# Optimization experiments

Measured on AMD Instinct MI355X. Metric: run time of the kernel, lower is better.

The kernel has to match this reference:

```python
import jax, jax.numpy as jnp
import numpy as np

BN_EPS = 1e-5

def _conv(x, w, b, pad):
    # x: [B,C,H,W], w: [O,I,kh,kw] -> [B,O,H,W]
    y = jax.lax.conv_general_dilated(x, w, window_strides=(1, 1),
                                     padding=[(pad, pad), (pad, pad)],
                                     dimension_numbers=("NCHW", "OIHW", "NCHW"))
    return y + b[None, :, None, None]

def setup_inputs() -> dict:
    key = jax.random.key(0)
    ks = jax.random.split(key, 5)
    B, Cin, H, W = 2, 256, 80, 80
    Ck, Cv, Cout = 128, 256, 256
    std = 0.02  # matches torch normal_(0, 0.02) init
    return {
        "x": jax.random.normal(ks[0], (B, Cin, H, W), jnp.float32),
        "wk": std * jax.random.normal(ks[1], (Ck, Cin, 1, 1), jnp.float32),
        "bk": jnp.zeros((Ck,), jnp.float32),
        "gamma": jnp.ones((Ck,), jnp.float32),
        "beta": jnp.zeros((Ck,), jnp.float32),
        "rmean": jnp.zeros((Ck,), jnp.float32),
        "rvar": jnp.ones((Ck,), jnp.float32),
        "wv": std * jax.random.normal(ks[2], (Cv, Cin, 3, 3), jnp.float32),
        "bv": jnp.zeros((Cv,), jnp.float32),
        "ww": std * jax.random.normal(ks[3], (Cout, Cv, 1, 1), jnp.float32),
        "bw": jnp.zeros((Cout,), jnp.float32),
    }

def reference(x, wk, bk, gamma, beta, rmean, rvar, wv, bv, ww, bw):
    B, Cin, H, W = x.shape
    Ck, Cv = wk.shape[0], wv.shape[0]
    N = H * W

    # f_key == f_query (shared module): 1x1 conv + BatchNorm (inference stats)
    kq = _conv(x, wk, bk, pad=0)                      # [B,Ck,H,W]
    inv = gamma / jnp.sqrt(rvar + BN_EPS)
    kq = kq * inv[None, :, None, None] + (beta - rmean * inv)[None, :, None, None]
    kq = kq.reshape(B, Ck, N)                          # key layout [B,Ck,N]

    # f_value: 3x3 conv
    value = _conv(x, wv, bv, pad=1).reshape(B, Cv, N)  # [B,Cv,N]

    # sim_map = query^T @ key -> [B,N,N], full softmax over last dim
    sim = jnp.einsum("bcn,bcm->bnm", kq, kq)
    sim = jax.nn.softmax(sim, axis=-1)

    # context = sim @ value^T -> [B,N,Cv] -> [B,Cv,H,W]
    ctx = jnp.einsum("bnm,bcm->bcn", sim, value).reshape(B, Cv, H, W)

    out = _conv(ctx, ww, bw, pad=0) + x                # residual
    return out
```

## Files before the change

### kernel.cpp

```cpp
#include <hip/hip_runtime.h>
#include <math.h>

#define NB   2
#define CIN  256
#define IMH  80
#define IMW  80
#define NPIX (IMH*IMW)
#define CK   128
#define CVC  256
#define COUTC 256
#define BN_EPS 1e-5f
#define HP   82
#define WP   82
#define SPLIT 2
#define NC   (NPIX / SPLIT / 64)
#define NMC  (NPIX / 64)

typedef short sx8 __attribute__((ext_vector_type(8)));
typedef short sx4 __attribute__((ext_vector_type(4)));
typedef float f32x4 __attribute__((ext_vector_type(4)));

__device__ __forceinline__ short f2bf(float f) {
    unsigned u = __builtin_bit_cast(unsigned, f);
    u += 0x7fffu + ((u >> 16) & 1u);
    return (short)(u >> 16);
}
__device__ __forceinline__ float bf2f(short s) {
    unsigned u = ((unsigned)(unsigned short)s) << 16;
    return __builtin_bit_cast(float, u);
}

__global__ __launch_bounds__(256) void pad_kernel(const float* __restrict__ x,
                                                  short* __restrict__ xpad)
{
    __shared__ short T[64][258];
    const int tid = threadIdx.x;
    const int n0  = blockIdx.x * 64;
    const int b   = blockIdx.y;
    const float* xb = x + (size_t)b * CIN * NPIX;

    #pragma unroll 4
    for (int i = 0; i < 64; ++i) {
        int e = tid + i * 256;
        int pix = e & 63, c = e >> 6;
        T[pix][c] = f2bf(xb[(size_t)c * NPIX + n0 + pix]);
    }
    __syncthreads();
    #pragma unroll
    for (int i = 0; i < 8; ++i) {
        int e   = tid + i * 256;
        int pix = e >> 5;
        int cp  = (e & 31) * 8;
        int np  = n0 + pix;
        int hp  = np / IMW + 1, wp = np % IMW + 1;
        sx8 v = *(const sx8*)&T[pix][cp];
        *(sx8*)&xpad[(((size_t)b * HP + hp) * WP + wp) * CIN + cp] = v;
    }
}

__global__ __launch_bounds__(256) void wvt_kernel(const float* __restrict__ wv,
                                                  short* __restrict__ wvt)
{
    int idx = blockIdx.x * 256 + threadIdx.x;
    int tap = idx >> 16;
    int cv  = (idx >> 8) & 255;
    int c   = idx & 255;
    wvt[idx] = f2bf(wv[((size_t)cv * CIN + c) * 9 + tap]);
}

__global__ __launch_bounds__(256) void wwb_kernel(const float* __restrict__ ww,
                                                  short* __restrict__ wwb)
{
    int idx = blockIdx.x * 256 + threadIdx.x;
    wwb[idx] = f2bf(ww[idx]);
}

__global__ __launch_bounds__(256) void wkb_kernel(
    const float* __restrict__ wk, const float* __restrict__ bk,
    const float* __restrict__ gamma, const float* __restrict__ beta,
    const float* __restrict__ rmean, const float* __restrict__ rvar,
    short* __restrict__ wkb, float* __restrict__ bias2)
{
    int idx = blockIdx.x * 256 + threadIdx.x;
    int ck = idx >> 8;
    float inv = gamma[ck] * rsqrtf(rvar[ck] + BN_EPS);
    wkb[idx] = f2bf(wk[idx] * inv);
    if (idx < CK) {
        float invi = gamma[idx] * rsqrtf(rvar[idx] + BN_EPS);
        bias2[idx] = (bk[idx] - rmean[idx]) * invi + beta[idx];
    }
}

__global__ __launch_bounds__(256) void kq_kernel(
    const short* __restrict__ xpad, const short* __restrict__ wkb,
    const float* __restrict__ bias2, short* __restrict__ kqT)
{
    __shared__ short T[64][136];
    const int tid  = threadIdx.x;
    const int wid  = tid >> 6;
    const int lane = tid & 63;
    const int l15  = lane & 15;
    const int quad = lane >> 4;
    const int n0 = blockIdx.x * 64;
    const int b  = blockIdx.y;
    const short* xb = xpad + (size_t)b * HP * WP * CIN;
    const int ck0 = wid * 32;

    const short* brow[4];
    #pragma unroll
    for (int nt = 0; nt < 4; ++nt) {
        int n = n0 + nt * 16 + l15;
        int hp = n / IMW + 1, wp = n % IMW + 1;
        brow[nt] = xb + ((size_t)hp * WP + wp) * CIN;
    }

    f32x4 acc[2][4];
    #pragma unroll
    for (int at = 0; at < 2; ++at)
        #pragma unroll
        for (int nt = 0; nt < 4; ++nt)
            acc[at][nt] = (f32x4){0.f, 0.f, 0.f, 0.f};

    for (int kc = 0; kc < CIN / 32; ++kc) {
        sx8 af0 = *(const sx8*)&wkb[(size_t)(ck0 + l15) * CIN + kc * 32 + quad * 8];
        sx8 af1 = *(const sx8*)&wkb[(size_t)(ck0 + 16 + l15) * CIN + kc * 32 + quad * 8];
        #pragma unroll
        for (int nt = 0; nt < 4; ++nt) {
            sx8 bf = *(const sx8*)&brow[nt][kc * 32 + quad * 8];
            acc[0][nt] = __builtin_amdgcn_mfma_f32_16x16x32_bf16(af0, bf, acc[0][nt], 0, 0, 0);
            acc[1][nt] = __builtin_amdgcn_mfma_f32_16x16x32_bf16(af1, bf, acc[1][nt], 0, 0, 0);
        }
    }

    #pragma unroll
    for (int at = 0; at < 2; ++at) {
        f32x4 b4 = *(const f32x4*)&bias2[ck0 + at * 16 + quad * 4];
        #pragma unroll
        for (int nt = 0; nt < 4; ++nt)
            #pragma unroll
            for (int r = 0; r < 4; ++r)
                T[nt * 16 + l15][ck0 + at * 16 + quad * 4 + r] = f2bf(acc[at][nt][r] + b4[r]);
    }
    __syncthreads();
    #pragma unroll
    for (int it = 0; it < 4; ++it) {
        int e = tid + it * 256;
        int row = e >> 4, c8 = (e & 15) * 8;
        *(sx8*)&kqT[((size_t)b * NPIX + n0 + row) * CK + c8] = *(const sx8*)&T[row][c8];
    }
}

#define CSTRIDE 36
__global__ __launch_bounds__(256) void conv3_kernel(
    const short* __restrict__ xpad, const short* __restrict__ wvt,
    const float* __restrict__ bv, short* __restrict__ val)
{
    __shared__ __align__(16) short Xs[6 * 18 * CSTRIDE];

    const int tid  = threadIdx.x;
    const int wid  = tid >> 6;
    const int lane = tid & 63;
    const int l15  = lane & 15;
    const int quad = lane >> 4;

    const int rowT = blockIdx.x / 5, colT = blockIdx.x % 5;
    const int h0 = rowT * 4, w0 = colT * 16;
    const int cv0 = blockIdx.y * 64 + wid * 16;
    const int b   = blockIdx.z;

    const short* xb = xpad + (size_t)b * HP * WP * CIN;

    f32x4 acc[4];
    #pragma unroll
    for (int r = 0; r < 4; ++r) acc[r] = (f32x4){0.f, 0.f, 0.f, 0.f};

    for (int cc = 0; cc < CIN / 32; ++cc) {
        __syncthreads();
        #pragma unroll
        for (int i = 0; i < 2; ++i) {
            int e = tid + i * 256;
            if (e < 432) {
                int rc = e >> 2, l4 = e & 3;
                int row = rc / 18, col = rc % 18;
                sx8 v = *(const sx8*)&xb[(((size_t)(h0 + row)) * WP + (w0 + col)) * CIN + cc * 32 + l4 * 8];
                *(sx8*)&Xs[rc * CSTRIDE + l4 * 8] = v;
            }
        }
        __syncthreads();

        #pragma unroll
        for (int dw = 0; dw < 3; ++dw) {
            sx8 Bf[6];
            #pragma unroll
            for (int rr = 0; rr < 6; ++rr)
                Bf[rr] = *(const sx8*)&Xs[(rr * 18 + l15 + dw) * CSTRIDE + quad * 8];
            #pragma unroll
            for (int dh = 0; dh < 3; ++dh) {
                int tap = dh * 3 + dw;
                sx8 Af = *(const sx8*)&wvt[((size_t)(tap * 256 + cv0 + l15)) * CIN + cc * 32 + quad * 8];
                #pragma unroll
                for (int r = 0; r < 4; ++r)
                    acc[r] = __builtin_amdgcn_mfma_f32_16x16x32_bf16(Af, Bf[r + dh], acc[r], 0, 0, 0);
            }
        }
    }

    f32x4 bvv = *(const f32x4*)&bv[cv0 + quad * 4];
    #pragma unroll
    for (int r = 0; r < 4; ++r) {
        int n = (h0 + r) * IMW + w0 + l15;
        #pragma unroll
        for (int reg = 0; reg < 4; ++reg) {
            int cv = cv0 + quad * 4 + reg;
            val[((size_t)b * CVC + cv) * NPIX + n] = f2bf(acc[r][reg] + bvv[reg]);
        }
    }
}

__global__ __launch_bounds__(256) void repack_kernel(const short* __restrict__ val,
                                                     short* __restrict__ valF)
{
    const int tid = threadIdx.x;
    const int mc  = blockIdx.x;
    const int b   = blockIdx.y;
    const int mg  = tid & 7;
    const int cvb = tid >> 3;
    const int s2  = mg >> 2, qm = mg & 3;
    #pragma unroll
    for (int p = 0; p < 8; ++p) {
        int cv = cvb + p * 32;
        sx8 v = *(const sx8*)&val[((size_t)b * CVC + cv) * NPIX + mc * 64 + mg * 8];
        size_t d = ((((size_t)(b * NMC + mc) * 16 + (cv >> 4)) * 2 + s2) * 4 + qm) * 128
                 + (cv & 15) * 8;
        *(sx8*)&valF[d] = v;
    }
}

#define TQ 64
#define TK 64
#define KS_LD 136
#define PS_LD 66

__global__ __launch_bounds__(256) void attn_kernel(
    const short* __restrict__ kqT, const short* __restrict__ valF,
    short* __restrict__ opart, float* __restrict__ mpart, float* __restrict__ lpart)
{
    __shared__ __align__(16) short Ks[2][TK][KS_LD];
    __shared__ __align__(16) short Pb[2][TQ][PS_LD];
    __shared__ float arow[2][TQ];

    const int tid  = threadIdx.x;
    const int wid  = tid >> 6;
    const int lane = tid & 63;
    const int l15  = lane & 15;
    const int quad = lane >> 4;

    const int blk = blockIdx.x;
    const int b   = blk & 1;
    const int sp  = (blk >> 1) & 1;
    const int n0  = (blk >> 2) * TQ;
    const int mb  = sp * (NPIX / SPLIT);

    const short* kqb = kqT + (size_t)b * NPIX * CK;
    const short* vbase = valF + ((size_t)(b * NMC + sp * NC) * 16 + wid * 4) * 1024
                              + (size_t)lane * 8;

    const int srow = tid >> 4;
    const int sc8  = (tid & 15) * 8;

    sx8 qf[4];
    #pragma unroll
    for (int s = 0; s < 4; ++s)
        qf[s] = *(const sx8*)&kqb[(size_t)(n0 + wid * 16 + l15) * CK + s * 32 + quad * 8];

    sx8 kreg[4];
    #pragma unroll
    for (int p = 0; p < 4; ++p)
        kreg[p] = *(const sx8*)&kqb[(size_t)(mb + srow + p * 16) * CK + sc8];
    #pragma unroll
    for (int p = 0; p < 4; ++p)
        *(sx8*)&Ks[0][srow + p * 16][sc8] = kreg[p];

    sx8 vreg[8];
    #pragma unroll
    for (int s2 = 0; s2 < 2; ++s2)
        #pragma unroll
        for (int ct = 0; ct < 4; ++ct)
            vreg[s2 * 4 + ct] = *(const sx8*)&vbase[ct * 1024 + s2 * 512];

    float mq = -1e30f, lq = 0.f;
    f32x4 acc[4][4];
    #pragma unroll
    for (int qt = 0; qt < 4; ++qt)
        #pragma unroll
        for (int ct = 0; ct < 4; ++ct)
            acc[qt][ct] = (f32x4){0.f, 0.f, 0.f, 0.f};

    __syncthreads();

    for (int i = 0; i < NC; ++i) {
        const int cur = i & 1;
        const int m0  = mb + i * TK;

        if (i + 1 < NC) {
            #pragma unroll
            for (int p = 0; p < 4; ++p)
                kreg[p] = *(const sx8*)&kqb[(size_t)(m0 + TK + srow + p * 16) * CK + sc8];
        }

        f32x4 st[4];
        #pragma unroll
        for (int t2 = 0; t2 < 4; ++t2) st[t2] = (f32x4){0.f, 0.f, 0.f, 0.f};
        #pragma unroll
        for (int s = 0; s < 4; ++s) {
            #pragma unroll
            for (int t2 = 0; t2 < 4; ++t2) {
                sx8 af = *(const sx8*)&Ks[cur][t2 * 16 + l15][s * 32 + quad * 8];
                st[t2] = __builtin_amdgcn_mfma_f32_16x16x32_bf16(af, qf[s], st[t2], 0, 0, 0);
            }
        }

        float mx = st[0][0];
        #pragma unroll
        for (int t2 = 0; t2 < 4; ++t2)
            #pragma unroll
            for (int r = 0; r < 4; ++r)
                mx = fmaxf(mx, st[t2][r]);
        mx = fmaxf(mx, __shfl_xor(mx, 16));
        mx = fmaxf(mx, __shfl_xor(mx, 32));
        float mnew = fmaxf(mq, mx);
        float alpha = __expf(mq - mnew);
        mq = mnew;
        float sum = 0.f;
        #pragma unroll
        for (int t2 = 0; t2 < 4; ++t2) {
            #pragma unroll
            for (int r = 0; r < 4; ++r) {
                float p = __expf(st[t2][r] - mnew);
                st[t2][r] = p;
                sum += p;
            }
        }
        sum += __shfl_xor(sum, 16);
        sum += __shfl_xor(sum, 32);
        lq = lq * alpha + sum;

        if (quad == 0) arow[cur][wid * 16 + l15] = alpha;
        #pragma unroll
        for (int t2 = 0; t2 < 4; ++t2) {
            sx4 pw;
            #pragma unroll
            for (int r = 0; r < 4; ++r) pw[r] = f2bf(st[t2][r]);
            *(sx4*)&Pb[cur][wid * 16 + l15][t2 * 16 + quad * 4] = pw;
        }

        if (i + 1 < NC) {
            #pragma unroll
            for (int p = 0; p < 4; ++p)
                *(sx8*)&Ks[cur ^ 1][srow + p * 16][sc8] = kreg[p];
        }
        __syncthreads();

        #pragma unroll
        for (int qt = 0; qt < 4; ++qt) {
            f32x4 a4 = *(const f32x4*)&arow[cur][qt * 16 + quad * 4];
            #pragma unroll
            for (int ct = 0; ct < 4; ++ct)
                acc[qt][ct] *= a4;
        }
        #pragma unroll
        for (int s2 = 0; s2 < 2; ++s2) {
            sx8 pa[4];
            #pragma unroll
            for (int qt = 0; qt < 4; ++qt)
                pa[qt] = *(const sx8*)&Pb[cur][qt * 16 + l15][s2 * 32 + quad * 8];
            #pragma unroll
            for (int ct = 0; ct < 4; ++ct) {
                #pragma unroll
                for (int qt = 0; qt < 4; ++qt)
                    acc[qt][ct] = __builtin_amdgcn_mfma_f32_16x16x32_bf16(pa[qt], vreg[s2 * 4 + ct], acc[qt][ct], 0, 0, 0);
            }
        }

        if (i + 1 < NC) {
            #pragma unroll
            for (int s2 = 0; s2 < 2; ++s2)
                #pragma unroll
                for (int ct = 0; ct < 4; ++ct)
                    vreg[s2 * 4 + ct] = *(const sx8*)&vbase[(size_t)(i + 1) * 16384 + ct * 1024 + s2 * 512];
        }
    }

    size_t obase = (size_t)(sp * NB + b) * NPIX + n0;
    #pragma unroll
    for (int qt = 0; qt < 4; ++qt)
        #pragma unroll
        for (int ct = 0; ct < 4; ++ct) {
            int cv = wid * 64 + ct * 16 + l15;
            #pragma unroll
            for (int r = 0; r < 4; ++r)
                opart[(obase + qt * 16 + quad * 4 + r) * CVC + cv] = f2bf(acc[qt][ct][r]);
        }
    if (quad == 0) {
        mpart[obase + wid * 16 + l15] = mq;
        lpart[obase + wid * 16 + l15] = lq;
    }
}

#define BS_LD 40
__global__ __launch_bounds__(256) void out_kernel(
    const short* __restrict__ opart, const float* __restrict__ mpart,
    const float* __restrict__ lpart, const short* __restrict__ wwb,
    const float* __restrict__ bw, const float* __restrict__ x,
    float* __restrict__ out)
{
    __shared__ __align__(16) short Bs[64][BS_LD];
    __shared__ float w0s[64], w1s[64];

    const int tid  = threadIdx.x;
    const int wid  = tid >> 6;
    const int lane = tid & 63;
    const int l15  = lane & 15;
    const int quad = lane >> 4;

    const int n0  = blockIdx.x * 64;
    const int co0 = blockIdx.y * 64 + wid * 16;
    const int b   = blockIdx.z;

    if (tid < 64) {
        int n = n0 + tid;
        size_t r0 = (size_t)b * NPIX + n;
        size_t r1 = (size_t)(NB + b) * NPIX + n;
        float m0 = mpart[r0], m1 = mpart[r1];
        float l0 = lpart[r0], l1 = lpart[r1];
        float M  = fmaxf(m0, m1);
        float w0 = __expf(m0 - M), w1 = __expf(m1 - M);
        float rinv = 1.f / (w0 * l0 + w1 * l1);
        w0s[tid] = w0 * rinv;
        w1s[tid] = w1 * rinv;
    }

    const int srow = tid >> 2;
    const int sc8  = (tid & 3) * 8;
    const short* o0p = opart + ((size_t)b * NPIX + n0 + srow) * CVC + sc8;
    const short* o1p = o0p + (size_t)NB * NPIX * CVC;

    f32x4 acc[4];
    #pragma unroll
    for (int nt = 0; nt < 4; ++nt) acc[nt] = (f32x4){0.f, 0.f, 0.f, 0.f};

    for (int cc = 0; cc < CVC / 32; ++cc) {
        __syncthreads();
        {
            sx8 a = *(const sx8*)&o0p[cc * 32];
            sx8 bq = *(const sx8*)&o1p[cc * 32];
            float w0 = w0s[srow], w1 = w1s[srow];
            sx8 o;
            #pragma unroll
            for (int j = 0; j < 8; ++j)
                o[j] = f2bf(bf2f(a[j]) * w0 + bf2f(bq[j]) * w1);
            *(sx8*)&Bs[srow][sc8] = o;
        }
        __syncthreads();
        sx8 af = *(const sx8*)&wwb[(size_t)(co0 + l15) * CVC + cc * 32 + quad * 8];
        #pragma unroll
        for (int nt = 0; nt < 4; ++nt) {
            sx8 bf = *(const sx8*)&Bs[nt * 16 + l15][quad * 8];
            acc[nt] = __builtin_amdgcn_mfma_f32_16x16x32_bf16(af, bf, acc[nt], 0, 0, 0);
        }
    }

    f32x4 bv4 = *(const f32x4*)&bw[co0 + quad * 4];
    #pragma unroll
    for (int nt = 0; nt < 4; ++nt) {
        #pragma unroll
        for (int r = 0; r < 4; ++r) {
            int co = co0 + quad * 4 + r;
            int n  = n0 + nt * 16 + l15;
            size_t gi = ((size_t)b * COUTC + co) * NPIX + n;
            out[gi] = acc[nt][r] + bv4[r] + x[gi];
        }
    }
}

extern "C" void kernel_launch(void* const* d_in, const int* in_sizes, int n_in,
                              void* d_out, int out_size, void* d_ws, size_t ws_size,
                              hipStream_t stream)
{
    const float* x     = (const float*)d_in[0];
    const float* wk    = (const float*)d_in[1];
    const float* bk    = (const float*)d_in[2];
    const float* gamma = (const float*)d_in[3];
    const float* beta  = (const float*)d_in[4];
    const float* rmean = (const float*)d_in[5];
    const float* rvar  = (const float*)d_in[6];
    const float* wv    = (const float*)d_in[7];
    const float* bv    = (const float*)d_in[8];
    const float* ww    = (const float*)d_in[9];
    const float* bw    = (const float*)d_in[10];
    float* out = (float*)d_out;

    short* xpad  = (short*)d_ws;
    short* wvt   = xpad + (size_t)NB * HP * WP * CIN;
    short* vbuf  = wvt + (size_t)9 * CVC * CIN;
    short* opart = xpad;
    short* wwb   = vbuf + (size_t)NB * CVC * NPIX;
    short* wkb   = wwb  + (size_t)COUTC * CVC;
    short* kqT   = wkb  + (size_t)CK * CIN;
    short* valF  = kqT  + (size_t)NB * NPIX * CK;
    float* bias2 = (float*)(valF + (size_t)NB * NPIX * CVC);
    float* mpart = bias2 + CK;
    float* lpart = mpart + (size_t)SPLIT * NB * NPIX;

    hipMemsetAsync(xpad, 0, (size_t)NB * HP * WP * CIN * sizeof(short), stream);

    pad_kernel   <<<dim3(NPIX/64, NB),          256, 0, stream>>>(x, xpad);
    wvt_kernel   <<<(9*CVC*CIN)/256,            256, 0, stream>>>(wv, wvt);
    wwb_kernel   <<<(COUTC*CVC)/256,            256, 0, stream>>>(ww, wwb);
    wkb_kernel   <<<(CK*CIN)/256,               256, 0, stream>>>(wk, bk, gamma, beta, rmean, rvar, wkb, bias2);
    kq_kernel    <<<dim3(NPIX/64, NB),          256, 0, stream>>>(xpad, wkb, bias2, kqT);
    conv3_kernel <<<dim3(100, CVC/64,      NB), 256, 0, stream>>>(xpad, wvt, bv, vbuf);
    repack_kernel<<<dim3(NMC, NB),              256, 0, stream>>>(vbuf, valF);
    attn_kernel  <<<NB * SPLIT * (NPIX / TQ),   256, 0, stream>>>(kqT, valF, opart, mpart, lpart);
    out_kernel   <<<dim3(100, COUTC/64,    NB), 256, 0, stream>>>(opart, mpart, lpart, wwb, bw, x, out);
}
```

Before: 273.6 us.

## Split attention keys four ways, fuse value repack into conv, skip no-op rescales

The key dimension of the attention is split four ways instead of two, doubling the attention grid for better CU occupancy. The out kernel now merges four partial results. The conv3 kernel writes values directly in the fragment layout the attention kernel reads, which removes the separate repack kernel and its intermediate buffer. Softmax exponentials switch to exp2 with a folded log2e multiply. The accumulator rescale is skipped when every alpha in the wave equals one, and LDS padding strides are changed. The extra split costs more partial-output memory traffic and merge work, and the direct conv3 stores are scattered 2-byte writes.

```diff
diff --git a/kernel.cpp b/kernel.cpp
--- a/kernel.cpp
+++ b/kernel.cpp
@@ -12,9 +12,10 @@
 #define BN_EPS 1e-5f
 #define HP   82
 #define WP   82
-#define SPLIT 2
+#define SPLIT 4
 #define NC   (NPIX / SPLIT / 64)
 #define NMC  (NPIX / 64)
+#define LOG2E 1.4426950408889634f
 
 typedef short sx8 __attribute__((ext_vector_type(8)));
 typedef short sx4 __attribute__((ext_vector_type(4)));
@@ -153,7 +154,7 @@
 #define CSTRIDE 36
 __global__ __launch_bounds__(256) void conv3_kernel(
     const short* __restrict__ xpad, const short* __restrict__ wvt,
-    const float* __restrict__ bv, short* __restrict__ val)
+    const float* __restrict__ bv, short* __restrict__ valF)
 {
     __shared__ __align__(16) short Xs[6 * 18 * CSTRIDE];
 
@@ -206,40 +207,22 @@
     }
 
     f32x4 bvv = *(const f32x4*)&bv[cv0 + quad * 4];
+    const int cvt = cv0 >> 4;
     #pragma unroll
     for (int r = 0; r < 4; ++r) {
-        int n = (h0 + r) * IMW + w0 + l15;
-        #pragma unroll
-        for (int reg = 0; reg < 4; ++reg) {
-            int cv = cv0 + quad * 4 + reg;
-            val[((size_t)b * CVC + cv) * NPIX + n] = f2bf(acc[r][reg] + bvv[reg]);
-        }
-    }
-}
-
-__global__ __launch_bounds__(256) void repack_kernel(const short* __restrict__ val,
-                                                     short* __restrict__ valF)
-{
-    const int tid = threadIdx.x;
-    const int mc  = blockIdx.x;
-    const int b   = blockIdx.y;
-    const int mg  = tid & 7;
-    const int cvb = tid >> 3;
-    const int s2  = mg >> 2, qm = mg & 3;
-    #pragma unroll
-    for (int p = 0; p < 8; ++p) {
-        int cv = cvb + p * 32;
-        sx8 v = *(const sx8*)&val[((size_t)b * CVC + cv) * NPIX + mc * 64 + mg * 8];
-        size_t d = ((((size_t)(b * NMC + mc) * 16 + (cv >> 4)) * 2 + s2) * 4 + qm) * 128
-                 + (cv & 15) * 8;
-        *(sx8*)&valF[d] = v;
+        int n  = (h0 + r) * IMW + w0 + l15;
+        int mc = n >> 6, s2 = (n >> 5) & 1, qm = (n >> 3) & 3, mi = n & 7;
+        size_t base = ((((size_t)(b * NMC + mc) * 16 + cvt) * 2 + s2) * 4 + qm) * 128;
+        #pragma unroll
+        for (int reg = 0; reg < 4; ++reg)
+            valF[base + (quad * 4 + reg) * 8 + mi] = f2bf(acc[r][reg] + bvv[reg]);
     }
 }
 
 #define TQ 64
 #define TK 64
-#define KS_LD 136
-#define PS_LD 66
+#define KS_LD 132
+#define PS_LD 72
 
 __global__ __launch_bounds__(256) void attn_kernel(
     const short* __restrict__ kqT, const short* __restrict__ valF,
@@ -257,8 +240,8 @@
 
     const int blk = blockIdx.x;
     const int b   = blk & 1;
-    const int sp  = (blk >> 1) & 1;
-    const int n0  = (blk >> 2) * TQ;
+    const int sp  = (blk >> 1) & 3;
+    const int n0  = (blk >> 3) * TQ;
     const int mb  = sp * (NPIX / SPLIT);
 
     const short* kqb = kqT + (size_t)b * NPIX * CK;
@@ -329,14 +312,15 @@
         mx = fmaxf(mx, __shfl_xor(mx, 16));
         mx = fmaxf(mx, __shfl_xor(mx, 32));
         float mnew = fmaxf(mq, mx);
-        float alpha = __expf(mq - mnew);
+        float mL = mnew * LOG2E;
+        float alpha = exp2f(fmaf(mq, LOG2E, -mL));
         mq = mnew;
         float sum = 0.f;
         #pragma unroll
         for (int t2 = 0; t2 < 4; ++t2) {
             #pragma unroll
             for (int r = 0; r < 4; ++r) {
-                float p = __expf(st[t2][r] - mnew);
+                float p = exp2f(fmaf(st[t2][r], LOG2E, -mL));
                 st[t2][r] = p;
                 sum += p;
             }
@@ -361,12 +345,22 @@
         }
         __syncthreads();
 
-        #pragma unroll
-        for (int qt = 0; qt < 4; ++qt) {
-            f32x4 a4 = *(const f32x4*)&arow[cur][qt * 16 + quad * 4];
-            #pragma unroll
-            for (int ct = 0; ct < 4; ++ct)
-                acc[qt][ct] *= a4;
+        {
+            f32x4 a4[4];
+            #pragma unroll
+            for (int qt = 0; qt < 4; ++qt)
+                a4[qt] = *(const f32x4*)&arow[cur][qt * 16 + quad * 4];
+            float amin = fminf(fminf(a4[0][0], a4[0][1]), fminf(a4[0][2], a4[0][3]));
+            #pragma unroll
+            for (int qt = 1; qt < 4; ++qt)
+                amin = fminf(amin, fminf(fminf(a4[qt][0], a4[qt][1]), fminf(a4[qt][2], a4[qt][3])));
+            if (__any(amin < 1.0f)) {
+                #pragma unroll
+                for (int qt = 0; qt < 4; ++qt)
+                    #pragma unroll
+                    for (int ct = 0; ct < 4; ++ct)
+                        acc[qt][ct] *= a4[qt];
+            }
         }
         #pragma unroll
         for (int s2 = 0; s2 < 2; ++s2) {
@@ -415,7 +409,7 @@
     float* __restrict__ out)
 {
     __shared__ __align__(16) short Bs[64][BS_LD];
-    __shared__ float w0s[64], w1s[64];
+    __shared__ float wms[SPLIT][64];
 
     const int tid  = threadIdx.x;
     const int wid  = tid >> 6;
@@ -429,21 +423,30 @@
 
     if (tid < 64) {
         int n = n0 + tid;
-        size_t r0 = (size_t)b * NPIX + n;
-        size_t r1 = (size_t)(NB + b) * NPIX + n;
-        float m0 = mpart[r0], m1 = mpart[r1];
-        float l0 = lpart[r0], l1 = lpart[r1];
-        float M  = fmaxf(m0, m1);
-        float w0 = __expf(m0 - M), w1 = __expf(m1 - M);
-        float rinv = 1.f / (w0 * l0 + w1 * l1);
-        w0s[tid] = w0 * rinv;
-        w1s[tid] = w1 * rinv;
+        float m[SPLIT], l[SPLIT];
+        #pragma unroll
+        for (int s = 0; s < SPLIT; ++s) {
+            size_t r = (size_t)(s * NB + b) * NPIX + n;
+            m[s] = mpart[r];
+            l[s] = lpart[r];
+        }
+        float M = m[0];
+        #pragma unroll
+        for (int s = 1; s < SPLIT; ++s) M = fmaxf(M, m[s]);
+        float w[SPLIT], denom = 0.f;
+        #pragma unroll
+        for (int s = 0; s < SPLIT; ++s) { w[s] = __expf(m[s] - M); denom += w[s] * l[s]; }
+        float rinv = 1.f / denom;
+        #pragma unroll
+        for (int s = 0; s < SPLIT; ++s) wms[s][tid] = w[s] * rinv;
     }
 
     const int srow = tid >> 2;
     const int sc8  = (tid & 3) * 8;
-    const short* o0p = opart + ((size_t)b * NPIX + n0 + srow) * CVC + sc8;
-    const short* o1p = o0p + (size_t)NB * NPIX * CVC;
+    const short* op[SPLIT];
+    #pragma unroll
+    for (int s = 0; s < SPLIT; ++s)
+        op[s] = opart + ((size_t)(s * NB + b) * NPIX + n0 + srow) * CVC + sc8;
 
     f32x4 acc[4];
     #pragma unroll
@@ -452,13 +455,20 @@
     for (int cc = 0; cc < CVC / 32; ++cc) {
         __syncthreads();
         {
-            sx8 a = *(const sx8*)&o0p[cc * 32];
-            sx8 bq = *(const sx8*)&o1p[cc * 32];
-            float w0 = w0s[srow], w1 = w1s[srow];
+            float w[SPLIT];
+            #pragma unroll
+            for (int s = 0; s < SPLIT; ++s) w[s] = wms[s][srow];
+            sx8 ov[SPLIT];
+            #pragma unroll
+            for (int s = 0; s < SPLIT; ++s) ov[s] = *(const sx8*)&op[s][cc * 32];
             sx8 o;
             #pragma unroll
-            for (int j = 0; j < 8; ++j)
-                o[j] = f2bf(bf2f(a[j]) * w0 + bf2f(bq[j]) * w1);
+            for (int j = 0; j < 8; ++j) {
+                float v = bf2f(ov[0][j]) * w[0];
+                #pragma unroll
+                for (int s = 1; s < SPLIT; ++s) v = fmaf(bf2f(ov[s][j]), w[s], v);
+                o[j] = f2bf(v);
+            }
             *(sx8*)&Bs[srow][sc8] = o;
         }
         __syncthreads();
@@ -500,11 +510,10 @@
     const float* bw    = (const float*)d_in[10];
     float* out = (float*)d_out;
 
-    short* xpad  = (short*)d_ws;
+    short* opart = (short*)d_ws;
+    short* xpad  = opart;
     short* wvt   = xpad + (size_t)NB * HP * WP * CIN;
-    short* vbuf  = wvt + (size_t)9 * CVC * CIN;
-    short* opart = xpad;
-    short* wwb   = vbuf + (size_t)NB * CVC * NPIX;
+    short* wwb   = opart + (size_t)SPLIT * NB * NPIX * CVC;
     short* wkb   = wwb  + (size_t)COUTC * CVC;
     short* kqT   = wkb  + (size_t)CK * CIN;
     short* valF  = kqT  + (size_t)NB * NPIX * CK;
@@ -519,8 +528,7 @@
     wwb_kernel   <<<(COUTC*CVC)/256,            256, 0, stream>>>(ww, wwb);
     wkb_kernel   <<<(CK*CIN)/256,               256, 0, stream>>>(wk, bk, gamma, beta, rmean, rvar, wkb, bias2);
     kq_kernel    <<<dim3(NPIX/64, NB),          256, 0, stream>>>(xpad, wkb, bias2, kqT);
-    conv3_kernel <<<dim3(100, CVC/64,      NB), 256, 0, stream>>>(xpad, wvt, bv, vbuf);
-    repack_kernel<<<dim3(NMC, NB),              256, 0, stream>>>(vbuf, valF);
+    conv3_kernel <<<dim3(100, CVC/64,      NB), 256, 0, stream>>>(xpad, wvt, bv, valF);
     attn_kernel  <<<NB * SPLIT * (NPIX / TQ),   256, 0, stream>>>(kqT, valF, opart, mpart, lpart);
     out_kernel   <<<dim3(100, COUTC/64,    NB), 256, 0, stream>>>(opart, mpart, lpart, wwb, bw, x, out);
 }
```

Result: slower. 280.6 us (+2.6%).
